# Optimization experiments

Measured on AMD Instinct MI355X. Metric: run time of the kernel, lower is better.

The kernel has to match this reference:

```python
import jax, jax.numpy as jnp
import numpy as np

N_MC = 32
DT = 0.1
HIDDEN = 64
PROSPECTIVE_STEPS = 3
# scan_steps=3 -> first 3 of the hard-coded velocities
VELOCITIES = np.array([[0.2, 0.0], [0.0, 0.2], [0.15, 0.15]], dtype=np.float32)


def linear_interp_1d(x, out_size):
    """F.interpolate(mode='linear', align_corners=False) on last axis. x: [..., N]."""
    n = x.shape[-1]
    scale = n / out_size
    pos = (jnp.arange(out_size, dtype=x.dtype) + 0.5) * scale - 0.5
    pos = jnp.clip(pos, 0.0, n - 1)
    lo = jnp.floor(pos).astype(jnp.int32)
    hi = jnp.minimum(lo + 1, n - 1)
    w = pos - lo.astype(x.dtype)
    return x[..., lo] * (1.0 - w) + x[..., hi] * w


def setup_inputs() -> dict:
    key = jax.random.key(0)
    ks = jax.random.split(key, 8)
    B = 16384
    image = jax.random.uniform(ks[0], (B, 28, 28), dtype=jnp.float32)
    s = 1.0 / np.sqrt(N_MC)
    W_ff = jax.random.normal(ks[1], (N_MC, N_MC), dtype=jnp.float32) * s
    W_fb = jax.random.normal(ks[2], (N_MC, N_MC), dtype=jnp.float32) * s
    W_vel = jax.random.normal(ks[3], (N_MC, 2), dtype=jnp.float32) * s
    Wc1 = jax.random.normal(ks[4], (HIDDEN, 4 * N_MC), dtype=jnp.float32) * (1.0 / np.sqrt(4 * N_MC))
    bc1 = jnp.zeros((HIDDEN,), dtype=jnp.float32)
    Wc2 = jax.random.normal(ks[5], (10, HIDDEN), dtype=jnp.float32) * (1.0 / np.sqrt(HIDDEN))
    bc2 = jnp.zeros((10,), dtype=jnp.float32)
    return {"image": image, "W_ff": W_ff, "W_fb": W_fb, "W_vel": W_vel,
            "Wc1": Wc1, "bc1": bc1, "Wc2": Wc2, "bc2": bc2}


def _column_features(image, W_ff, W_fb, W_vel):
    B = image.shape[0]
    flat = image.reshape(B, -1)                       # [B, 784]
    flat_t = jnp.swapaxes(image, 1, 2).reshape(B, -1)  # transpose(0,1) per image
    sensory = linear_interp_1d(flat, N_MC) * 80.0     # [B, n_mc]
    topdown = linear_interp_1d(flat_t, N_MC) * 40.0   # [B, n_mc]

    r6 = jnp.zeros_like(sensory)                      # reset_state per image
    y_fb = jax.nn.relu(topdown @ W_fb.T)              # top-down feedback drive
    for v in VELOCITIES:                              # fixed 3-step scan
        vel_in = W_vel @ jnp.asarray(v)               # [n_mc]
        for _ in range(PROSPECTIVE_STEPS):            # fixed 3 prospective steps
            pred = r6 @ W_fb.T                        # top-down prediction of sensory drive
            eps_pos = jax.nn.relu(sensory - pred)
            eps_neg = jax.nn.relu(pred - sensory)
            y_ff = jax.nn.relu((eps_pos - eps_neg) @ W_ff.T)
            r6 = r6 + DT * (-r6 + y_ff + y_fb + vel_in)  # leaky L6 integrator
    feature = jnp.concatenate([y_ff, y_fb, r6, eps_pos + eps_neg], axis=-1)  # [B, 4*n_mc]
    return feature


def reference(image, W_ff, W_fb, W_vel, Wc1, bc1, Wc2, bc2):
    feature = jax.lax.stop_gradient(_column_features(image, W_ff, W_fb, W_vel))
    h = jax.nn.gelu(feature @ Wc1.T + bc1, approximate=False)
    logits = h @ Wc2.T + bc2                          # [B, 10]
    return logits
```

## Files before the change

kernel.cpp:

```cpp
#include <hip/hip_runtime.h>
#include <math.h>

typedef _Float16 f16x8 __attribute__((ext_vector_type(8)));
typedef float    f32x4 __attribute__((ext_vector_type(4)));

#define SCRW 132
#define IMG_F 784
#define CHUNK_F 3136

typedef __attribute__((address_space(3))) void lds_void;
typedef const __attribute__((address_space(1))) void glb_void;

__device__ __forceinline__ f32x4 mfma16(f16x8 a, f16x8 b, f32x4 c) {
  return __builtin_amdgcn_mfma_f32_16x16x32_f16(a, b, c, 0, 0, 0);
}

__device__ __forceinline__ void splitP(const float* p, f16x8& hi, f16x8& lo) {
  const f32x4* q = (const f32x4*)p;
  f32x4 a0 = q[0], a1 = q[1];
#pragma unroll
  for (int j = 0; j < 4; ++j) {
    _Float16 h0 = (_Float16)a0[j], h1 = (_Float16)a1[j];
    hi[j] = h0; hi[j + 4] = h1;
    lo[j]     = (_Float16)(a0[j] - (float)h0);
    lo[j + 4] = (_Float16)(a1[j] - (float)h1);
  }
}

__device__ __forceinline__ void splitS(const float* p, int stride, f16x8& hi, f16x8& lo) {
#pragma unroll
  for (int j = 0; j < 8; ++j) {
    float x = p[j * stride];
    _Float16 h = (_Float16)x;
    hi[j] = h;
    lo[j] = (_Float16)(x - (float)h);
  }
}

__device__ __forceinline__ f16x8 bfrag8(const float* p) {
  const f32x4* q = (const f32x4*)p;
  f32x4 w0 = q[0], w1 = q[1];
  f16x8 b;
#pragma unroll
  for (int j = 0; j < 4; ++j) { b[j] = (_Float16)w0[j]; b[j + 4] = (_Float16)w1[j]; }
  return b;
}

__device__ __forceinline__ void load_chunk(const float* gsrc, float* lbase, int l) {
#pragma unroll
  for (int i = 0; i < 12; ++i)
    __builtin_amdgcn_global_load_lds((glb_void*)(gsrc + i * 256 + l * 4),
                                     (lds_void*)(lbase + i * 256), 16, 0, 0);
  __builtin_amdgcn_global_load_lds((glb_void*)(gsrc + 3072 + l),
                                   (lds_void*)(lbase + 3072), 4, 0, 0);
}

__global__ __launch_bounds__(256) void mnist_cols(
    const float* __restrict__ img,  const float* __restrict__ Wff,
    const float* __restrict__ Wfb,  const float* __restrict__ Wvel,
    const float* __restrict__ Wc1,  const float* __restrict__ bc1,
    const float* __restrict__ Wc2,  const float* __restrict__ bc2,
    float* __restrict__ out) {
  __shared__ float img_lds[4][CHUNK_F];
  __shared__ float scr_all[4][16 * SCRW];

  const int tid = threadIdx.x;
  const int wv = tid >> 6, l = tid & 63;
  const int g = l >> 4, c0 = l & 15, c1 = c0 + 16;
  float* scr  = scr_all[wv];
  float* ibuf = img_lds[wv];
  const int s0 = blockIdx.x * 64 + wv * 16;

  const float pos0 = 24.5f * (float)c0 + 11.75f;
  const float pos1 = 24.5f * (float)c1 + 11.75f;
  const int lo0 = (int)pos0, lo1 = (int)pos1;
  const float w0 = pos0 - (float)lo0, w1 = pos1 - (float)lo1;
  const int ta0 = (lo0 % 28) * 28 + lo0 / 28;
  const int tb0 = ((lo0 + 1) % 28) * 28 + (lo0 + 1) / 28;
  const int ta1 = (lo1 % 28) * 28 + lo1 / 28;
  const int tb1 = ((lo1 + 1) % 28) * 28 + (lo1 + 1) / 28;

  f16x8 bfbh0, bfbl0, bfbh1, bfbl1, bffh0, bffl0, bffh1, bffl1;
  splitP(Wfb + c0 * 32 + g * 8, bfbh0, bfbl0);
  splitP(Wfb + c1 * 32 + g * 8, bfbh1, bfbl1);
  splitP(Wff + c0 * 32 + g * 8, bffh0, bffl0);
  splitP(Wff + c1 * 32 + g * 8, bffh1, bffl1);
  f16x8 afbh0, afbl0, afbh1, afbl1;
  splitS(Wfb + g * 256 + c0,      32, afbh0, afbl0);
  splitS(Wfb + g * 256 + c0 + 16, 32, afbh1, afbl1);
  const float wva0 = Wvel[c0 * 2], wva1 = Wvel[c0 * 2 + 1];
  const float wvb0 = Wvel[c1 * 2], wvb1 = Wvel[c1 * 2 + 1];

  load_chunk(img + (size_t)s0 * IMG_F, ibuf, l);

  const f32x4 zero = {0.f, 0.f, 0.f, 0.f};
  f32x4 m00 = mfma16(afbh0, bffl0, mfma16(afbl0, bffh0, mfma16(afbh0, bffh0, zero)));
  f32x4 m01 = mfma16(afbh0, bffl1, mfma16(afbl0, bffh1, mfma16(afbh0, bffh1, zero)));
  f32x4 m10 = mfma16(afbh1, bffl0, mfma16(afbl1, bffh0, mfma16(afbh1, bffh0, zero)));
  f32x4 m11 = mfma16(afbh1, bffl1, mfma16(afbl1, bffh1, mfma16(afbh1, bffh1, zero)));
#pragma unroll
  for (int r = 0; r < 4; ++r) {
    scr[(g * 4 + r) * 32 + c0]            = m00[r];
    scr[(g * 4 + r) * 32 + c0 + 16]       = m01[r];
    scr[(16 + g * 4 + r) * 32 + c0]       = m10[r];
    scr[(16 + g * 4 + r) * 32 + c0 + 16]  = m11[r];
  }
  f16x8 mbh0, mbl0, mbh1, mbl1;
  splitS(scr + g * 256 + c0,      32, mbh0, mbl0);
  splitS(scr + g * 256 + c0 + 16, 32, mbh1, mbl1);

  float sens[4][2] = {}, td[4][2] = {};
#pragma unroll
  for (int c = 0; c < 4; ++c) {
    asm volatile("s_waitcnt vmcnt(0)" ::: "memory");
    __builtin_amdgcn_sched_barrier(0);
    if (g == c) {
#pragma unroll
      for (int r = 0; r < 4; ++r) {
        const float* base = ibuf + r * IMG_F;
        float sa0 = base[lo0], sa1 = base[lo0 + 1];
        float sb0 = base[lo1], sb1 = base[lo1 + 1];
        float t00 = base[ta0], t01 = base[tb0];
        float t10 = base[ta1], t11 = base[tb1];
        sens[r][0] = (sa0 * (1.0f - w0) + sa1 * w0) * 80.0f;
        sens[r][1] = (sb0 * (1.0f - w1) + sb1 * w1) * 80.0f;
        td[r][0]   = (t00 * (1.0f - w0) + t01 * w0) * 40.0f;
        td[r][1]   = (t10 * (1.0f - w1) + t11 * w1) * 40.0f;
      }
    }
    if (c < 3) load_chunk(img + (size_t)(s0 + (c + 1) * 4) * IMG_F, ibuf, l);
  }

  f16x8 ahi, alo;
#pragma unroll
  for (int r = 0; r < 4; ++r) {
    int row = (g * 4 + r) * SCRW;
    scr[row + c0] = td[r][0];
    scr[row + c1] = td[r][1];
  }
  splitP(scr + c0 * SCRW + g * 8, ahi, alo);
  f32x4 f0 = mfma16(ahi, bfbl0, mfma16(alo, bfbh0, mfma16(ahi, bfbh0, zero)));
  f32x4 f1 = mfma16(ahi, bfbl1, mfma16(alo, bfbh1, mfma16(ahi, bfbh1, zero)));
  float yfb[4][2];
#pragma unroll
  for (int r = 0; r < 4; ++r) { yfb[r][0] = fmaxf(f0[r], 0.f); yfb[r][1] = fmaxf(f1[r], 0.f); }

#pragma unroll
  for (int r = 0; r < 4; ++r) {
    int row = (g * 4 + r) * SCRW;
    scr[row + c0] = sens[r][0];
    scr[row + c1] = sens[r][1];
  }
  splitP(scr + c0 * SCRW + g * 8, ahi, alo);
  f32x4 sff0 = mfma16(ahi, bffl0, mfma16(alo, bffh0, mfma16(ahi, bffh0, zero)));
  f32x4 sff1 = mfma16(ahi, bffl1, mfma16(alo, bffh1, mfma16(ahi, bffh1, zero)));

  float r6[4][2] = {}, d[4][2] = {}, yff[4][2] = {};
  const float VX[3] = {0.2f, 0.0f, 0.15f};
  const float VY[3] = {0.0f, 0.2f, 0.15f};
#pragma unroll
  for (int v = 0; v < 3; ++v) {
    float vin[2];
    vin[0] = wva0 * VX[v] + wva1 * VY[v];
    vin[1] = wvb0 * VX[v] + wvb1 * VY[v];
#pragma unroll
    for (int st = 0; st < 3; ++st) {
#pragma unroll
      for (int r = 0; r < 4; ++r) {
        int row = (g * 4 + r) * SCRW;
        scr[row + c0] = -r6[r][0];
        scr[row + c1] = -r6[r][1];
      }
      splitP(scr + c0 * SCRW + g * 8, ahi, alo);
      f32x4 y0 = mfma16(ahi, mbl0, mfma16(alo, mbh0, mfma16(ahi, mbh0, sff0)));
      f32x4 y1 = mfma16(ahi, mbl1, mfma16(alo, mbh1, mfma16(ahi, mbh1, sff1)));
      if (v == 2 && st == 2) {
        f32x4 t0 = mfma16(ahi, bfbl0, mfma16(alo, bfbh0, mfma16(ahi, bfbh0, zero)));
        f32x4 t1 = mfma16(ahi, bfbl1, mfma16(alo, bfbh1, mfma16(ahi, bfbh1, zero)));
#pragma unroll
        for (int r = 0; r < 4; ++r) { d[r][0] = sens[r][0] + t0[r]; d[r][1] = sens[r][1] + t1[r]; }
      }
#pragma unroll
      for (int r = 0; r < 4; ++r) {
        yff[r][0] = fmaxf(y0[r], 0.f);
        yff[r][1] = fmaxf(y1[r], 0.f);
        r6[r][0] += 0.1f * (yff[r][0] - r6[r][0] + yfb[r][0] + vin[0]);
        r6[r][1] += 0.1f * (yff[r][1] - r6[r][1] + yfb[r][1] + vin[1]);
      }
    }
  }

#pragma unroll
  for (int r = 0; r < 4; ++r) {
    int row = (g * 4 + r) * SCRW;
    scr[row +      c0] = yff[r][0];        scr[row +      c1] = yff[r][1];
    scr[row + 32 + c0] = yfb[r][0];        scr[row + 32 + c1] = yfb[r][1];
    scr[row + 64 + c0] = r6[r][0];         scr[row + 64 + c1] = r6[r][1];
    scr[row + 96 + c0] = fabsf(d[r][0]);   scr[row + 96 + c1] = fabsf(d[r][1]);
  }
  f32x4 acc0 = zero, acc1 = zero, acc2 = zero, acc3 = zero;
#pragma unroll
  for (int kb = 0; kb < 4; ++kb) {
    f16x8 fhi, flo;
    splitP(scr + c0 * SCRW + kb * 32 + g * 8, fhi, flo);
    const int ko = kb * 32 + g * 8;
    f16x8 b0 = bfrag8(Wc1 + (size_t)(c0)      * 128 + ko);
    f16x8 b1 = bfrag8(Wc1 + (size_t)(16 + c0) * 128 + ko);
    f16x8 b2 = bfrag8(Wc1 + (size_t)(32 + c0) * 128 + ko);
    f16x8 b3 = bfrag8(Wc1 + (size_t)(48 + c0) * 128 + ko);
    acc0 = mfma16(flo, b0, mfma16(fhi, b0, acc0));
    acc1 = mfma16(flo, b1, mfma16(fhi, b1, acc1));
    acc2 = mfma16(flo, b2, mfma16(fhi, b2, acc2));
    acc3 = mfma16(flo, b3, mfma16(fhi, b3, acc3));
  }
  float h[4][4];
  const float B0 = bc1[c0], B1 = bc1[16 + c0], B2 = bc1[32 + c0], B3 = bc1[48 + c0];
#pragma unroll
  for (int r = 0; r < 4; ++r) {
    float x0 = acc0[r] + B0, x1 = acc1[r] + B1, x2 = acc2[r] + B2, x3 = acc3[r] + B3;
    h[r][0] = 0.5f * x0 * (1.0f + erff(x0 * 0.70710678118654752f));
    h[r][1] = 0.5f * x1 * (1.0f + erff(x1 * 0.70710678118654752f));
    h[r][2] = 0.5f * x2 * (1.0f + erff(x2 * 0.70710678118654752f));
    h[r][3] = 0.5f * x3 * (1.0f + erff(x3 * 0.70710678118654752f));
  }

#pragma unroll
  for (int r = 0; r < 4; ++r) {
    int row = (g * 4 + r) * SCRW;
#pragma unroll
    for (int nb = 0; nb < 4; ++nb) scr[row + nb * 16 + c0] = h[r][nb];
  }
  f32x4 accL = zero;
#pragma unroll
  for (int kb = 0; kb < 2; ++kb) {
    f16x8 hhi, hlo;
    splitP(scr + c0 * SCRW + kb * 32 + g * 8, hhi, hlo);
    f16x8 b;
    if (c0 < 10) {
      b = bfrag8(Wc2 + (size_t)c0 * 64 + kb * 32 + g * 8);
    } else {
#pragma unroll
      for (int j = 0; j < 8; ++j) b[j] = (_Float16)0.f;
    }
    accL = mfma16(hlo, b, mfma16(hhi, b, accL));
  }
  if (c0 < 10) {
    const float bb = bc2[c0];
#pragma unroll
    for (int r = 0; r < 4; ++r)
      out[(size_t)(s0 + g * 4 + r) * 10 + c0] = accL[r] + bb;
  }
}

extern "C" void kernel_launch(void* const* d_in, const int* in_sizes, int n_in,
                              void* d_out, int out_size, void* d_ws, size_t ws_size,
                              hipStream_t stream) {
  const float* img  = (const float*)d_in[0];
  const float* Wff  = (const float*)d_in[1];
  const float* Wfb  = (const float*)d_in[2];
  const float* Wvel = (const float*)d_in[3];
  const float* Wc1  = (const float*)d_in[4];
  const float* bc1  = (const float*)d_in[5];
  const float* Wc2  = (const float*)d_in[6];
  const float* bc2  = (const float*)d_in[7];
  float* out = (float*)d_out;
  const int B = in_sizes[0] / 784;
  const int grid = B / 64;
  hipLaunchKernelGGL(mnist_cols, dim3(grid), dim3(256), 0, stream,
                     img, Wff, Wfb, Wvel, Wc1, bc1, Wc2, bc2, out);
}
```

Before: 24.36 us.

## Split image interpolation into separate streaming kernel writing to workspace

Moves the image loading and linear interpolation out of the fused column kernel into a dedicated kernel. That kernel streams one image per wave step, double-buffered in LDS, and writes the sensory and top-down vectors to workspace. The main kernel then reads these small vectors instead of holding large LDS image chunks, which frees LDS for higher occupancy in both stages. The cost is a second launch plus a round-trip of the intermediate vectors through global memory.

```diff
diff --git a/kernel.cpp b/kernel.cpp
--- a/kernel.cpp
+++ b/kernel.cpp
@@ -5,8 +5,7 @@
 typedef float    f32x4 __attribute__((ext_vector_type(4)));
 
 #define SCRW 132
-#define IMG_F 784
-#define CHUNK_F 3136
+#define G_IMG 8
 
 typedef __attribute__((address_space(3))) void lds_void;
 typedef const __attribute__((address_space(1))) void glb_void;
@@ -46,39 +45,86 @@
   return b;
 }
 
-__device__ __forceinline__ void load_chunk(const float* gsrc, float* lbase, int l) {
-#pragma unroll
-  for (int i = 0; i < 12; ++i)
-    __builtin_amdgcn_global_load_lds((glb_void*)(gsrc + i * 256 + l * 4),
-                                     (lds_void*)(lbase + i * 256), 16, 0, 0);
-  __builtin_amdgcn_global_load_lds((glb_void*)(gsrc + 3072 + l),
-                                   (lds_void*)(lbase + 3072), 4, 0, 0);
+__global__ __launch_bounds__(256) void interp_k(const float* __restrict__ img,
+                                                float* __restrict__ sensW,
+                                                float* __restrict__ tdW) {
+  __shared__ float buf[4][2][800];
+  const int tid = threadIdx.x, wv = tid >> 6, l = tid & 63;
+  const int u = l & 31, half = l >> 5;
+  const int img0 = (blockIdx.x * 4 + wv) * G_IMG;
+
+  const float pos = 24.5f * (float)u + 11.75f;
+  const int lo = (int)pos;
+  const float w = pos - (float)lo;
+  const int ta = (lo % 28) * 28 + lo / 28;
+  const int tb = ((lo + 1) % 28) * 28 + (lo + 1) / 28;
+  const int p0 = half ? ta : lo;
+  const int p1 = half ? tb : (lo + 1);
+  const float scale = half ? 40.0f : 80.0f;
+  float* outp = half ? tdW : sensW;
+
+  {
+    const float* src = img + (size_t)img0 * 784;
+    float* dst = &buf[wv][0][0];
+#pragma unroll
+    for (int j = 0; j < 3; ++j)
+      __builtin_amdgcn_global_load_lds((glb_void*)(src + j * 256 + l * 4),
+                                       (lds_void*)(dst + j * 256), 16, 0, 0);
+    if (l < 4)
+      __builtin_amdgcn_global_load_lds((glb_void*)(src + 768 + l * 4),
+                                       (lds_void*)(dst + 768), 16, 0, 0);
+  }
+
+  float v[G_IMG];
+#pragma unroll
+  for (int i = 0; i < G_IMG; ++i) {
+    if (i + 1 < G_IMG) {
+      const float* src = img + (size_t)(img0 + i + 1) * 784;
+      float* dst = &buf[wv][(i + 1) & 1][0];
+#pragma unroll
+      for (int j = 0; j < 3; ++j)
+        __builtin_amdgcn_global_load_lds((glb_void*)(src + j * 256 + l * 4),
+                                         (lds_void*)(dst + j * 256), 16, 0, 0);
+      if (l < 4)
+        __builtin_amdgcn_global_load_lds((glb_void*)(src + 768 + l * 4),
+                                         (lds_void*)(dst + 768), 16, 0, 0);
+      asm volatile("s_waitcnt vmcnt(4)" ::: "memory");
+    } else {
+      asm volatile("s_waitcnt vmcnt(0)" ::: "memory");
+    }
+    __builtin_amdgcn_sched_barrier(0);
+    const float* b = &buf[wv][i & 1][0];
+    float v0 = b[p0], v1 = b[p1];
+    v[i] = (v0 * (1.0f - w) + v1 * w) * scale;
+  }
+#pragma unroll
+  for (int i = 0; i < G_IMG; ++i)
+    outp[(size_t)(img0 + i) * 32 + u] = v[i];
 }
 
 __global__ __launch_bounds__(256) void mnist_cols(
-    const float* __restrict__ img,  const float* __restrict__ Wff,
-    const float* __restrict__ Wfb,  const float* __restrict__ Wvel,
-    const float* __restrict__ Wc1,  const float* __restrict__ bc1,
-    const float* __restrict__ Wc2,  const float* __restrict__ bc2,
-    float* __restrict__ out) {
-  __shared__ float img_lds[4][CHUNK_F];
+    const float* __restrict__ sensW, const float* __restrict__ tdW,
+    const float* __restrict__ Wff,  const float* __restrict__ Wfb,
+    const float* __restrict__ Wvel, const float* __restrict__ Wc1,
+    const float* __restrict__ bc1,  const float* __restrict__ Wc2,
+    const float* __restrict__ bc2,  float* __restrict__ out) {
   __shared__ float scr_all[4][16 * SCRW];
 
   const int tid = threadIdx.x;
   const int wv = tid >> 6, l = tid & 63;
   const int g = l >> 4, c0 = l & 15, c1 = c0 + 16;
-  float* scr  = scr_all[wv];
-  float* ibuf = img_lds[wv];
+  float* scr = scr_all[wv];
   const int s0 = blockIdx.x * 64 + wv * 16;
 
-  const float pos0 = 24.5f * (float)c0 + 11.75f;
-  const float pos1 = 24.5f * (float)c1 + 11.75f;
-  const int lo0 = (int)pos0, lo1 = (int)pos1;
-  const float w0 = pos0 - (float)lo0, w1 = pos1 - (float)lo1;
-  const int ta0 = (lo0 % 28) * 28 + lo0 / 28;
-  const int tb0 = ((lo0 + 1) % 28) * 28 + (lo0 + 1) / 28;
-  const int ta1 = (lo1 % 28) * 28 + lo1 / 28;
-  const int tb1 = ((lo1 + 1) % 28) * 28 + (lo1 + 1) / 28;
+  float sens[4][2], td[4][2];
+#pragma unroll
+  for (int r = 0; r < 4; ++r) {
+    const int row = s0 + g * 4 + r;
+    sens[r][0] = sensW[row * 32 + c0];
+    sens[r][1] = sensW[row * 32 + c1];
+    td[r][0]   = tdW[row * 32 + c0];
+    td[r][1]   = tdW[row * 32 + c1];
+  }
 
   f16x8 bfbh0, bfbl0, bfbh1, bfbl1, bffh0, bffl0, bffh1, bffl1;
   splitP(Wfb + c0 * 32 + g * 8, bfbh0, bfbl0);
@@ -91,8 +137,6 @@
   const float wva0 = Wvel[c0 * 2], wva1 = Wvel[c0 * 2 + 1];
   const float wvb0 = Wvel[c1 * 2], wvb1 = Wvel[c1 * 2 + 1];
 
-  load_chunk(img + (size_t)s0 * IMG_F, ibuf, l);
-
   const f32x4 zero = {0.f, 0.f, 0.f, 0.f};
   f32x4 m00 = mfma16(afbh0, bffl0, mfma16(afbl0, bffh0, mfma16(afbh0, bffh0, zero)));
   f32x4 m01 = mfma16(afbh0, bffl1, mfma16(afbl0, bffh1, mfma16(afbh0, bffh1, zero)));
@@ -100,36 +144,14 @@
   f32x4 m11 = mfma16(afbh1, bffl1, mfma16(afbl1, bffh1, mfma16(afbh1, bffh1, zero)));
 #pragma unroll
   for (int r = 0; r < 4; ++r) {
-    scr[(g * 4 + r) * 32 + c0]            = m00[r];
-    scr[(g * 4 + r) * 32 + c0 + 16]       = m01[r];
-    scr[(16 + g * 4 + r) * 32 + c0]       = m10[r];
-    scr[(16 + g * 4 + r) * 32 + c0 + 16]  = m11[r];
+    scr[(g * 4 + r) * 32 + c0]           = m00[r];
+    scr[(g * 4 + r) * 32 + c0 + 16]      = m01[r];
+    scr[(16 + g * 4 + r) * 32 + c0]      = m10[r];
+    scr[(16 + g * 4 + r) * 32 + c0 + 16] = m11[r];
   }
   f16x8 mbh0, mbl0, mbh1, mbl1;
   splitS(scr + g * 256 + c0,      32, mbh0, mbl0);
   splitS(scr + g * 256 + c0 + 16, 32, mbh1, mbl1);
-
-  float sens[4][2] = {}, td[4][2] = {};
-#pragma unroll
-  for (int c = 0; c < 4; ++c) {
-    asm volatile("s_waitcnt vmcnt(0)" ::: "memory");
-    __builtin_amdgcn_sched_barrier(0);
-    if (g == c) {
-#pragma unroll
-      for (int r = 0; r < 4; ++r) {
-        const float* base = ibuf + r * IMG_F;
-        float sa0 = base[lo0], sa1 = base[lo0 + 1];
-        float sb0 = base[lo1], sb1 = base[lo1 + 1];
-        float t00 = base[ta0], t01 = base[tb0];
-        float t10 = base[ta1], t11 = base[tb1];
-        sens[r][0] = (sa0 * (1.0f - w0) + sa1 * w0) * 80.0f;
-        sens[r][1] = (sb0 * (1.0f - w1) + sb1 * w1) * 80.0f;
-        td[r][0]   = (t00 * (1.0f - w0) + t01 * w0) * 40.0f;
-        td[r][1]   = (t10 * (1.0f - w1) + t11 * w1) * 40.0f;
-      }
-    }
-    if (c < 3) load_chunk(img + (size_t)(s0 + (c + 1) * 4) * IMG_F, ibuf, l);
-  }
 
   f16x8 ahi, alo;
 #pragma unroll
@@ -265,7 +287,14 @@
   const float* bc2  = (const float*)d_in[7];
   float* out = (float*)d_out;
   const int B = in_sizes[0] / 784;
-  const int grid = B / 64;
-  hipLaunchKernelGGL(mnist_cols, dim3(grid), dim3(256), 0, stream,
-                     img, Wff, Wfb, Wvel, Wc1, bc1, Wc2, bc2, out);
-}
+
+  float* sensW = (float*)d_ws;
+  float* tdW   = sensW + (size_t)B * 32;
+
+  const int grid1 = B / (4 * G_IMG);
+  hipLaunchKernelGGL(interp_k, dim3(grid1), dim3(256), 0, stream, img, sensW, tdW);
+
+  const int grid2 = B / 64;
+  hipLaunchKernelGGL(mnist_cols, dim3(grid2), dim3(256), 0, stream,
+                     sensW, tdW, Wff, Wfb, Wvel, Wc1, bc1, Wc2, bc2, out);
+}
```

Measured after the change: 26.85 us. 1.1x slower.

## Transpose recurrence to feature-major MFMA layout and exchange state via ds_bpermute

Applied to the files above, without the earlier changes.

The recurrent loop now keeps features in the MFMA M dimension and samples in N. Each step rebuilds the r6 operand with ds_bpermute lane shuffles instead of writing to LDS scratch and reading it back. Interpolation is restructured so each lane handles one sample and computes all 8 of its features, plus a second sensory copy in the output layout. The aim is to take LDS round trips and waits off the 9-step serial chain, at the cost of extra gather loads and duplicated interpolation work.

```diff
diff --git a/kernel.cpp b/kernel.cpp
--- a/kernel.cpp
+++ b/kernel.cpp
@@ -5,14 +5,31 @@
 typedef float    f32x4 __attribute__((ext_vector_type(4)));
 
 #define SCRW 132
-#define IMG_F 784
-#define CHUNK_F 3136
+#define MLDW 33
 
 typedef __attribute__((address_space(3))) void lds_void;
 typedef const __attribute__((address_space(1))) void glb_void;
 
 __device__ __forceinline__ f32x4 mfma16(f16x8 a, f16x8 b, f32x4 c) {
   return __builtin_amdgcn_mfma_f32_16x16x32_f16(a, b, c, 0, 0, 0);
+}
+
+__device__ __forceinline__ void pack8(const float* v, f16x8& hi, f16x8& lo) {
+#pragma unroll
+  for (int j = 0; j < 8; ++j) {
+    _Float16 h = (_Float16)v[j];
+    hi[j] = h;
+    lo[j] = (_Float16)(v[j] - (float)h);
+  }
+}
+
+__device__ __forceinline__ f16x8 bfrag8(const float* p) {
+  const f32x4* q = (const f32x4*)p;
+  f32x4 w0 = q[0], w1 = q[1];
+  f16x8 b;
+#pragma unroll
+  for (int j = 0; j < 4; ++j) { b[j] = (_Float16)w0[j]; b[j + 4] = (_Float16)w1[j]; }
+  return b;
 }
 
 __device__ __forceinline__ void splitP(const float* p, f16x8& hi, f16x8& lo) {
@@ -27,25 +44,6 @@
   }
 }
 
-__device__ __forceinline__ void splitS(const float* p, int stride, f16x8& hi, f16x8& lo) {
-#pragma unroll
-  for (int j = 0; j < 8; ++j) {
-    float x = p[j * stride];
-    _Float16 h = (_Float16)x;
-    hi[j] = h;
-    lo[j] = (_Float16)(x - (float)h);
-  }
-}
-
-__device__ __forceinline__ f16x8 bfrag8(const float* p) {
-  const f32x4* q = (const f32x4*)p;
-  f32x4 w0 = q[0], w1 = q[1];
-  f16x8 b;
-#pragma unroll
-  for (int j = 0; j < 4; ++j) { b[j] = (_Float16)w0[j]; b[j + 4] = (_Float16)w1[j]; }
-  return b;
-}
-
 __device__ __forceinline__ void load_chunk(const float* gsrc, float* lbase, int l) {
 #pragma unroll
   for (int i = 0; i < 12; ++i)
@@ -55,166 +53,240 @@
                                    (lds_void*)(lbase + 3072), 4, 0, 0);
 }
 
-__global__ __launch_bounds__(256) void mnist_cols(
+__global__ __launch_bounds__(256) void mnist_fused(
     const float* __restrict__ img,  const float* __restrict__ Wff,
     const float* __restrict__ Wfb,  const float* __restrict__ Wvel,
     const float* __restrict__ Wc1,  const float* __restrict__ bc1,
     const float* __restrict__ Wc2,  const float* __restrict__ bc2,
     float* __restrict__ out) {
-  __shared__ float img_lds[4][CHUNK_F];
+  __shared__ float img_lds[4][784 * 4];
   __shared__ float scr_all[4][16 * SCRW];
 
   const int tid = threadIdx.x;
   const int wv = tid >> 6, l = tid & 63;
-  const int g = l >> 4, c0 = l & 15, c1 = c0 + 16;
+  const int g = l >> 4, c = l & 15;
   float* scr  = scr_all[wv];
+  float* Mlds = scr;
   float* ibuf = img_lds[wv];
   const int s0 = blockIdx.x * 64 + wv * 16;
-
-  const float pos0 = 24.5f * (float)c0 + 11.75f;
-  const float pos1 = 24.5f * (float)c1 + 11.75f;
-  const int lo0 = (int)pos0, lo1 = (int)pos1;
-  const float w0 = pos0 - (float)lo0, w1 = pos1 - (float)lo1;
-  const int ta0 = (lo0 % 28) * 28 + lo0 / 28;
-  const int tb0 = ((lo0 + 1) % 28) * 28 + (lo0 + 1) / 28;
-  const int ta1 = (lo1 % 28) * 28 + lo1 / 28;
-  const int tb1 = ((lo1 + 1) % 28) * 28 + (lo1 + 1) / 28;
-
-  f16x8 bfbh0, bfbl0, bfbh1, bfbl1, bffh0, bffl0, bffh1, bffl1;
-  splitP(Wfb + c0 * 32 + g * 8, bfbh0, bfbl0);
-  splitP(Wfb + c1 * 32 + g * 8, bfbh1, bfbl1);
-  splitP(Wff + c0 * 32 + g * 8, bffh0, bffl0);
-  splitP(Wff + c1 * 32 + g * 8, bffh1, bffl1);
-  f16x8 afbh0, afbl0, afbh1, afbl1;
-  splitS(Wfb + g * 256 + c0,      32, afbh0, afbl0);
-  splitS(Wfb + g * 256 + c0 + 16, 32, afbh1, afbl1);
-  const float wva0 = Wvel[c0 * 2], wva1 = Wvel[c0 * 2 + 1];
-  const float wvb0 = Wvel[c1 * 2], wvb1 = Wvel[c1 * 2 + 1];
-
-  load_chunk(img + (size_t)s0 * IMG_F, ibuf, l);
-
   const f32x4 zero = {0.f, 0.f, 0.f, 0.f};
-  f32x4 m00 = mfma16(afbh0, bffl0, mfma16(afbl0, bffh0, mfma16(afbh0, bffh0, zero)));
-  f32x4 m01 = mfma16(afbh0, bffl1, mfma16(afbl0, bffh1, mfma16(afbh0, bffh1, zero)));
-  f32x4 m10 = mfma16(afbh1, bffl0, mfma16(afbl1, bffh0, mfma16(afbh1, bffh0, zero)));
-  f32x4 m11 = mfma16(afbh1, bffl1, mfma16(afbl1, bffh1, mfma16(afbh1, bffh1, zero)));
+
+  f32x4 rff[4], rfb[4];
+  rff[0] = *(const f32x4*)(Wff + c * 32 + g * 8);
+  rff[1] = *(const f32x4*)(Wff + c * 32 + g * 8 + 4);
+  rff[2] = *(const f32x4*)(Wff + (16 + c) * 32 + g * 8);
+  rff[3] = *(const f32x4*)(Wff + (16 + c) * 32 + g * 8 + 4);
+  rfb[0] = *(const f32x4*)(Wfb + c * 32 + g * 8);
+  rfb[1] = *(const f32x4*)(Wfb + c * 32 + g * 8 + 4);
+  rfb[2] = *(const f32x4*)(Wfb + (16 + c) * 32 + g * 8);
+  rfb[3] = *(const f32x4*)(Wfb + (16 + c) * 32 + g * 8 + 4);
+  float rT0[8], rT1[8];
+#pragma unroll
+  for (int j = 0; j < 8; ++j) {
+    rT0[j] = Wfb[(g * 8 + j) * 32 + c];
+    rT1[j] = Wfb[(g * 8 + j) * 32 + 16 + c];
+  }
+  float2 wv0[4], wv1[4];
+#pragma unroll
+  for (int e = 0; e < 4; ++e) {
+    wv0[e] = ((const float2*)Wvel)[g * 4 + e];
+    wv1[e] = ((const float2*)Wvel)[16 + g * 4 + e];
+  }
+  __builtin_amdgcn_sched_barrier(0);
+
+  load_chunk(img + (size_t)s0 * 784, ibuf, l);
+
+  int loB[8], taB[8], tbB[8], loQ[8];
+  float wB[8], wQ[8];
+#pragma unroll
+  for (int j = 0; j < 8; ++j) {
+    int u = g * 8 + j;
+    float pos = 24.5f * (float)u + 11.75f;
+    loB[j] = (int)pos; wB[j] = pos - (float)loB[j];
+    int lt = loB[j];
+    taB[j] = (lt % 28) * 28 + lt / 28;
+    lt += 1;
+    tbB[j] = (lt % 28) * 28 + lt / 28;
+  }
+#pragma unroll
+  for (int e2 = 0; e2 < 8; ++e2) {
+    int u = (e2 >> 2) * 16 + g * 4 + (e2 & 3);
+    float pos = 24.5f * (float)u + 11.75f;
+    loQ[e2] = (int)pos; wQ[e2] = pos - (float)loQ[e2];
+  }
+
+  f16x8 bffh0, bffl0, bffh1, bffl1, bfbh0, bfbl0, bfbh1, bfbl1;
+  {
+    float t[8];
+#pragma unroll
+    for (int j = 0; j < 4; ++j) { t[j] = rff[0][j]; t[4 + j] = rff[1][j]; }
+    pack8(t, bffh0, bffl0);
+#pragma unroll
+    for (int j = 0; j < 4; ++j) { t[j] = rff[2][j]; t[4 + j] = rff[3][j]; }
+    pack8(t, bffh1, bffl1);
+#pragma unroll
+    for (int j = 0; j < 4; ++j) { t[j] = rfb[0][j]; t[4 + j] = rfb[1][j]; }
+    pack8(t, bfbh0, bfbl0);
+#pragma unroll
+    for (int j = 0; j < 4; ++j) { t[j] = rfb[2][j]; t[4 + j] = rfb[3][j]; }
+    pack8(t, bfbh1, bfbl1);
+  }
+  f16x8 aT0h, aT0l, aT1h, aT1l;
+  pack8(rT0, aT0h, aT0l);
+  pack8(rT1, aT1h, aT1l);
+
+  f32x4 m00 = mfma16(aT0h, bffl0, mfma16(aT0l, bffh0, mfma16(aT0h, bffh0, zero)));
+  f32x4 m01 = mfma16(aT0h, bffl1, mfma16(aT0l, bffh1, mfma16(aT0h, bffh1, zero)));
+  f32x4 m10 = mfma16(aT1h, bffl0, mfma16(aT1l, bffh0, mfma16(aT1h, bffh0, zero)));
+  f32x4 m11 = mfma16(aT1h, bffl1, mfma16(aT1l, bffh1, mfma16(aT1h, bffh1, zero)));
 #pragma unroll
   for (int r = 0; r < 4; ++r) {
-    scr[(g * 4 + r) * 32 + c0]            = m00[r];
-    scr[(g * 4 + r) * 32 + c0 + 16]       = m01[r];
-    scr[(16 + g * 4 + r) * 32 + c0]       = m10[r];
-    scr[(16 + g * 4 + r) * 32 + c0 + 16]  = m11[r];
-  }
-  f16x8 mbh0, mbl0, mbh1, mbl1;
-  splitS(scr + g * 256 + c0,      32, mbh0, mbl0);
-  splitS(scr + g * 256 + c0 + 16, 32, mbh1, mbl1);
-
-  float sens[4][2] = {}, td[4][2] = {};
-#pragma unroll
-  for (int c = 0; c < 4; ++c) {
+    Mlds[(g * 4 + r) * MLDW + c]            = m00[r];
+    Mlds[(g * 4 + r) * MLDW + 16 + c]       = m01[r];
+    Mlds[(16 + g * 4 + r) * MLDW + c]       = m10[r];
+    Mlds[(16 + g * 4 + r) * MLDW + 16 + c]  = m11[r];
+  }
+  f16x8 nMt0h, nMt0l, nMt1h, nMt1l;
+  {
+    float m[8];
+#pragma unroll
+    for (int j = 0; j < 8; ++j) m[j] = -Mlds[(g * 8 + j) * MLDW + c];
+    pack8(m, nMt0h, nMt0l);
+#pragma unroll
+    for (int j = 0; j < 8; ++j) m[j] = -Mlds[(g * 8 + j) * MLDW + 16 + c];
+    pack8(m, nMt1h, nMt1l);
+  }
+
+  float sB[8] = {}, tB[8] = {}, sQ[8] = {};
+#pragma unroll
+  for (int ch = 0; ch < 4; ++ch) {
     asm volatile("s_waitcnt vmcnt(0)" ::: "memory");
     __builtin_amdgcn_sched_barrier(0);
-    if (g == c) {
-#pragma unroll
-      for (int r = 0; r < 4; ++r) {
-        const float* base = ibuf + r * IMG_F;
-        float sa0 = base[lo0], sa1 = base[lo0 + 1];
-        float sb0 = base[lo1], sb1 = base[lo1 + 1];
-        float t00 = base[ta0], t01 = base[tb0];
-        float t10 = base[ta1], t11 = base[tb1];
-        sens[r][0] = (sa0 * (1.0f - w0) + sa1 * w0) * 80.0f;
-        sens[r][1] = (sb0 * (1.0f - w1) + sb1 * w1) * 80.0f;
-        td[r][0]   = (t00 * (1.0f - w0) + t01 * w0) * 40.0f;
-        td[r][1]   = (t10 * (1.0f - w1) + t11 * w1) * 40.0f;
-      }
-    }
-    if (c < 3) load_chunk(img + (size_t)(s0 + (c + 1) * 4) * IMG_F, ibuf, l);
-  }
-
-  f16x8 ahi, alo;
-#pragma unroll
-  for (int r = 0; r < 4; ++r) {
-    int row = (g * 4 + r) * SCRW;
-    scr[row + c0] = td[r][0];
-    scr[row + c1] = td[r][1];
-  }
-  splitP(scr + c0 * SCRW + g * 8, ahi, alo);
-  f32x4 f0 = mfma16(ahi, bfbl0, mfma16(alo, bfbh0, mfma16(ahi, bfbh0, zero)));
-  f32x4 f1 = mfma16(ahi, bfbl1, mfma16(alo, bfbh1, mfma16(ahi, bfbh1, zero)));
-  float yfb[4][2];
-#pragma unroll
-  for (int r = 0; r < 4; ++r) { yfb[r][0] = fmaxf(f0[r], 0.f); yfb[r][1] = fmaxf(f1[r], 0.f); }
-
-#pragma unroll
-  for (int r = 0; r < 4; ++r) {
-    int row = (g * 4 + r) * SCRW;
-    scr[row + c0] = sens[r][0];
-    scr[row + c1] = sens[r][1];
-  }
-  splitP(scr + c0 * SCRW + g * 8, ahi, alo);
-  f32x4 sff0 = mfma16(ahi, bffl0, mfma16(alo, bffh0, mfma16(ahi, bffh0, zero)));
-  f32x4 sff1 = mfma16(ahi, bffl1, mfma16(alo, bffh1, mfma16(ahi, bffh1, zero)));
-
-  float r6[4][2] = {}, d[4][2] = {}, yff[4][2] = {};
+    if ((c >> 2) == ch) {
+      const float* base = ibuf + (c & 3) * 784;
+#pragma unroll
+      for (int j = 0; j < 8; ++j) {
+        float a = base[loB[j]], b2 = base[loB[j] + 1];
+        sB[j] = (a + (b2 - a) * wB[j]) * 80.0f;
+      }
+#pragma unroll
+      for (int j = 0; j < 8; ++j) {
+        float a = base[taB[j]], b2 = base[tbB[j]];
+        tB[j] = (a + (b2 - a) * wB[j]) * 40.0f;
+      }
+#pragma unroll
+      for (int e2 = 0; e2 < 8; ++e2) {
+        float a = base[loQ[e2]], b2 = base[loQ[e2] + 1];
+        sQ[e2] = (a + (b2 - a) * wQ[e2]) * 80.0f;
+      }
+    }
+    if (ch < 3) load_chunk(img + (size_t)(s0 + (ch + 1) * 4) * 784, ibuf, l);
+  }
+
+  f16x8 snh, snl, tdh, tdl;
+  pack8(sB, snh, snl);
+  pack8(tB, tdh, tdl);
+  f32x4 SN0 = {sQ[0], sQ[1], sQ[2], sQ[3]};
+  f32x4 SN1 = {sQ[4], sQ[5], sQ[6], sQ[7]};
+
+  f32x4 SF0 = mfma16(bffh0, snh, zero);
+  SF0 += mfma16(bffl0, snh, mfma16(bffh0, snl, zero));
+  f32x4 SF1 = mfma16(bffh1, snh, zero);
+  SF1 += mfma16(bffl1, snh, mfma16(bffh1, snl, zero));
+  f32x4 YFB0 = mfma16(bfbh0, tdh, zero);
+  YFB0 += mfma16(bfbl0, tdh, mfma16(bfbh0, tdl, zero));
+  f32x4 YFB1 = mfma16(bfbh1, tdh, zero);
+  YFB1 += mfma16(bfbl1, tdh, mfma16(bfbh1, tdl, zero));
+#pragma unroll
+  for (int e = 0; e < 4; ++e) {
+    YFB0[e] = fmaxf(YFB0[e], 0.f);
+    YFB1[e] = fmaxf(YFB1[e], 0.f);
+  }
+
+  const int addrA = ((2 * (g & 1)) * 16 + c) * 4;
+  const int addrB = addrA + 64;
+  const bool hiG = (g >= 2);
+  f32x4 r6q0 = zero, r6q1 = zero;
+  f32x4 yf0 = zero, yf1 = zero, dq0 = zero, dq1 = zero;
   const float VX[3] = {0.2f, 0.0f, 0.15f};
   const float VY[3] = {0.0f, 0.2f, 0.15f};
 #pragma unroll
   for (int v = 0; v < 3; ++v) {
-    float vin[2];
-    vin[0] = wva0 * VX[v] + wva1 * VY[v];
-    vin[1] = wvb0 * VX[v] + wvb1 * VY[v];
+    f32x4 vq0, vq1;
+#pragma unroll
+    for (int e = 0; e < 4; ++e) {
+      vq0[e] = wv0[e].x * VX[v] + wv0[e].y * VY[v];
+      vq1[e] = wv1[e].x * VX[v] + wv1[e].y * VY[v];
+    }
 #pragma unroll
     for (int st = 0; st < 3; ++st) {
-#pragma unroll
-      for (int r = 0; r < 4; ++r) {
-        int row = (g * 4 + r) * SCRW;
-        scr[row + c0] = -r6[r][0];
-        scr[row + c1] = -r6[r][1];
-      }
-      splitP(scr + c0 * SCRW + g * 8, ahi, alo);
-      f32x4 y0 = mfma16(ahi, mbl0, mfma16(alo, mbh0, mfma16(ahi, mbh0, sff0)));
-      f32x4 y1 = mfma16(ahi, mbl1, mfma16(alo, mbh1, mfma16(ahi, mbh1, sff1)));
+      float t[8];
+#pragma unroll
+      for (int e = 0; e < 4; ++e) {
+        int q0i = __float_as_int(r6q0[e]), q1i = __float_as_int(r6q1[e]);
+        float a0 = __int_as_float(__builtin_amdgcn_ds_bpermute(addrA, q0i));
+        float a1 = __int_as_float(__builtin_amdgcn_ds_bpermute(addrA, q1i));
+        float b0 = __int_as_float(__builtin_amdgcn_ds_bpermute(addrB, q0i));
+        float b1 = __int_as_float(__builtin_amdgcn_ds_bpermute(addrB, q1i));
+        t[e]     = hiG ? a1 : a0;
+        t[4 + e] = hiG ? b1 : b0;
+      }
+      f16x8 bh, bl;
+      pack8(t, bh, bl);
+      f32x4 y0 = mfma16(nMt0h, bh, SF0);
+      y0 += mfma16(nMt0l, bh, mfma16(nMt0h, bl, zero));
+      f32x4 y1 = mfma16(nMt1h, bh, SF1);
+      y1 += mfma16(nMt1l, bh, mfma16(nMt1h, bl, zero));
       if (v == 2 && st == 2) {
-        f32x4 t0 = mfma16(ahi, bfbl0, mfma16(alo, bfbh0, mfma16(ahi, bfbh0, zero)));
-        f32x4 t1 = mfma16(ahi, bfbl1, mfma16(alo, bfbh1, mfma16(ahi, bfbh1, zero)));
-#pragma unroll
-        for (int r = 0; r < 4; ++r) { d[r][0] = sens[r][0] + t0[r]; d[r][1] = sens[r][1] + t1[r]; }
-      }
-#pragma unroll
-      for (int r = 0; r < 4; ++r) {
-        yff[r][0] = fmaxf(y0[r], 0.f);
-        yff[r][1] = fmaxf(y1[r], 0.f);
-        r6[r][0] += 0.1f * (yff[r][0] - r6[r][0] + yfb[r][0] + vin[0]);
-        r6[r][1] += 0.1f * (yff[r][1] - r6[r][1] + yfb[r][1] + vin[1]);
-      }
-    }
-  }
-
-#pragma unroll
-  for (int r = 0; r < 4; ++r) {
-    int row = (g * 4 + r) * SCRW;
-    scr[row +      c0] = yff[r][0];        scr[row +      c1] = yff[r][1];
-    scr[row + 32 + c0] = yfb[r][0];        scr[row + 32 + c1] = yfb[r][1];
-    scr[row + 64 + c0] = r6[r][0];         scr[row + 64 + c1] = r6[r][1];
-    scr[row + 96 + c0] = fabsf(d[r][0]);   scr[row + 96 + c1] = fabsf(d[r][1]);
-  }
+        f32x4 p0 = mfma16(bfbh0, bh, zero);
+        p0 += mfma16(bfbl0, bh, mfma16(bfbh0, bl, zero));
+        f32x4 p1 = mfma16(bfbh1, bh, zero);
+        p1 += mfma16(bfbl1, bh, mfma16(bfbh1, bl, zero));
+#pragma unroll
+        for (int e = 0; e < 4; ++e) { dq0[e] = SN0[e] - p0[e]; dq1[e] = SN1[e] - p1[e]; }
+      }
+#pragma unroll
+      for (int e = 0; e < 4; ++e) {
+        yf0[e] = fmaxf(y0[e], 0.f);
+        yf1[e] = fmaxf(y1[e], 0.f);
+        r6q0[e] += 0.1f * (yf0[e] - r6q0[e] + YFB0[e] + vq0[e]);
+        r6q1[e] += 0.1f * (yf1[e] - r6q1[e] + YFB1[e] + vq1[e]);
+      }
+    }
+  }
+
+  {
+    const int b0 = c * SCRW;
+#pragma unroll
+    for (int e = 0; e < 4; ++e) {
+      scr[b0 +       g * 4 + e] = yf0[e];
+      scr[b0 + 16  + g * 4 + e] = yf1[e];
+      scr[b0 + 32  + g * 4 + e] = YFB0[e];
+      scr[b0 + 48  + g * 4 + e] = YFB1[e];
+      scr[b0 + 64  + g * 4 + e] = r6q0[e];
+      scr[b0 + 80  + g * 4 + e] = r6q1[e];
+      scr[b0 + 96  + g * 4 + e] = fabsf(dq0[e]);
+      scr[b0 + 112 + g * 4 + e] = fabsf(dq1[e]);
+    }
+  }
+
   f32x4 acc0 = zero, acc1 = zero, acc2 = zero, acc3 = zero;
 #pragma unroll
   for (int kb = 0; kb < 4; ++kb) {
     f16x8 fhi, flo;
-    splitP(scr + c0 * SCRW + kb * 32 + g * 8, fhi, flo);
+    splitP(scr + c * SCRW + kb * 32 + g * 8, fhi, flo);
     const int ko = kb * 32 + g * 8;
-    f16x8 b0 = bfrag8(Wc1 + (size_t)(c0)      * 128 + ko);
-    f16x8 b1 = bfrag8(Wc1 + (size_t)(16 + c0) * 128 + ko);
-    f16x8 b2 = bfrag8(Wc1 + (size_t)(32 + c0) * 128 + ko);
-    f16x8 b3 = bfrag8(Wc1 + (size_t)(48 + c0) * 128 + ko);
+    f16x8 b0 = bfrag8(Wc1 + (size_t)(c)      * 128 + ko);
+    f16x8 b1 = bfrag8(Wc1 + (size_t)(16 + c) * 128 + ko);
+    f16x8 b2 = bfrag8(Wc1 + (size_t)(32 + c) * 128 + ko);
+    f16x8 b3 = bfrag8(Wc1 + (size_t)(48 + c) * 128 + ko);
     acc0 = mfma16(flo, b0, mfma16(fhi, b0, acc0));
     acc1 = mfma16(flo, b1, mfma16(fhi, b1, acc1));
     acc2 = mfma16(flo, b2, mfma16(fhi, b2, acc2));
     acc3 = mfma16(flo, b3, mfma16(fhi, b3, acc3));
   }
   float h[4][4];
-  const float B0 = bc1[c0], B1 = bc1[16 + c0], B2 = bc1[32 + c0], B3 = bc1[48 + c0];
+  const float B0 = bc1[c], B1 = bc1[16 + c], B2 = bc1[32 + c], B3 = bc1[48 + c];
 #pragma unroll
   for (int r = 0; r < 4; ++r) {
     float x0 = acc0[r] + B0, x1 = acc1[r] + B1, x2 = acc2[r] + B2, x3 = acc3[r] + B3;
@@ -223,32 +295,31 @@
     h[r][2] = 0.5f * x2 * (1.0f + erff(x2 * 0.70710678118654752f));
     h[r][3] = 0.5f * x3 * (1.0f + erff(x3 * 0.70710678118654752f));
   }
-
 #pragma unroll
   for (int r = 0; r < 4; ++r) {
     int row = (g * 4 + r) * SCRW;
 #pragma unroll
-    for (int nb = 0; nb < 4; ++nb) scr[row + nb * 16 + c0] = h[r][nb];
+    for (int nb = 0; nb < 4; ++nb) scr[row + nb * 16 + c] = h[r][nb];
   }
   f32x4 accL = zero;
 #pragma unroll
   for (int kb = 0; kb < 2; ++kb) {
     f16x8 hhi, hlo;
-    splitP(scr + c0 * SCRW + kb * 32 + g * 8, hhi, hlo);
+    splitP(scr + c * SCRW + kb * 32 + g * 8, hhi, hlo);
     f16x8 b;
-    if (c0 < 10) {
-      b = bfrag8(Wc2 + (size_t)c0 * 64 + kb * 32 + g * 8);
+    if (c < 10) {
+      b = bfrag8(Wc2 + (size_t)c * 64 + kb * 32 + g * 8);
     } else {
 #pragma unroll
       for (int j = 0; j < 8; ++j) b[j] = (_Float16)0.f;
     }
     accL = mfma16(hlo, b, mfma16(hhi, b, accL));
   }
-  if (c0 < 10) {
-    const float bb = bc2[c0];
+  if (c < 10) {
+    const float bb = bc2[c];
 #pragma unroll
     for (int r = 0; r < 4; ++r)
-      out[(size_t)(s0 + g * 4 + r) * 10 + c0] = accL[r] + bb;
+      out[(size_t)(s0 + g * 4 + r) * 10 + c] = accL[r] + bb;
   }
 }
 
@@ -266,6 +337,6 @@
   float* out = (float*)d_out;
   const int B = in_sizes[0] / 784;
   const int grid = B / 64;
-  hipLaunchKernelGGL(mnist_cols, dim3(grid), dim3(256), 0, stream,
+  hipLaunchKernelGGL(mnist_fused, dim3(grid), dim3(256), 0, stream,
                      img, Wff, Wfb, Wvel, Wc1, bc1, Wc2, bc2, out);
 }
```

After: 25.27 us. 3.8% more time.
